# Kernel optimization log

Measured on AMD Instinct MI355X. Metric: run time of the kernel, lower is better.

## Reference

```python
import jax, jax.numpy as jnp
import numpy as np

RADIUS = 3
DIAM = 2 * RADIUS + 1  # 7
NP = DIAM * DIAM       # 49 taps


def _cubic(d, a=-0.75):
    # torch bicubic kernel (a = -0.75)
    d = np.abs(d)
    return np.where(d <= 1, (a + 2) * d**3 - (a + 3) * d**2 + 1,
                    np.where(d < 2, a * d**3 - 5 * a * d**2 + 8 * a * d - 4 * a, 0.0))


def _resize_matrix(out_size, in_size):
    # dense [out,in] matrix reproducing torch F.interpolate bicubic, align_corners=False
    i = np.arange(out_size)
    x = (i + 0.5) * in_size / out_size - 0.5
    x0 = np.floor(x).astype(np.int64)
    t = x - x0
    W = np.zeros((out_size, in_size), np.float32)
    for k in range(-1, 3):
        w = _cubic(t - k)
        idx = np.clip(x0 + k, 0, in_size - 1)  # border replicate
        np.add.at(W, (i, idx), w.astype(np.float32))
    return jnp.asarray(W)


def _bicubic(x, GH, GW):
    B, C, H, W = x.shape
    Wh = _resize_matrix(GH, H)
    Ww = _resize_matrix(GW, W)
    return jnp.einsum('Hh,bchw,Ww->bcHW', Wh, x, Ww)


def _jbu(source, guidance, w1, b1, w2, b2, temp, sigma):
    # FeatUp JBULearnedRange.forward (eval mode: Dropout2d is identity)
    B, _, GH, GW = guidance.shape
    # range_proj: 1x1 conv -> GELU -> 1x1 conv
    q = jnp.einsum('kc,bchw->bkhw', w1, guidance) + b1[None, :, None, None]
    q = jax.nn.gelu(q, approximate=False)
    q = jnp.einsum('kc,bchw->bkhw', w2, q) + b2[None, :, None, None]  # [B,32,GH,GW]
    qp = jnp.pad(q, ((0, 0), (0, 0), (RADIUS, RADIUS), (RADIUS, RADIUS)), mode='reflect')
    # scores[b,p,h,w] = <key at center, key at offset p> (avoids B*32*49*H*W unfold)
    scores = jnp.stack([jnp.sum(qp[:, :, di:di + GH, dj:dj + GW] * q, axis=1)
                        for di in range(DIAM) for dj in range(DIAM)], axis=1)  # [B,49,GH,GW]
    t = jnp.clip(jnp.exp(temp), 1e-4, 1e4)
    range_kernel = jax.nn.softmax(t * scores, axis=1)
    dist = jnp.linspace(-1.0, 1.0, DIAM)
    gy, gx = jnp.meshgrid(dist, dist, indexing='ij')
    spatial_kernel = jnp.exp(-(gy**2 + gx**2) / (2.0 * sigma**2)).reshape(1, NP, 1, 1)
    k = range_kernel * spatial_kernel
    k = k / jnp.clip(jnp.sum(k, axis=1, keepdims=True), 1e-7, None)
    hr = _bicubic(source, GH, GW)
    hrp = jnp.pad(hr, ((0, 0), (0, 0), (RADIUS, RADIUS), (RADIUS, RADIUS)), mode='reflect')
    # AdaptiveConv: per-pixel 7x7 kernel applied to all channels
    out = jnp.zeros_like(hr)
    p_idx = 0
    for di in range(DIAM):
        for dj in range(DIAM):
            out = out + hrp[:, :, di:di + GH, dj:dj + GW] * k[:, p_idx][:, None]
            p_idx += 1
    return out


def _forward(x, guidance, linear_w, linear_b, w1s, b1s, w2s, b2s, temps, sigmas):
    f = (x @ linear_w.T + linear_b).reshape(-1, 3, 18, 18)
    for i in range(4):  # up1..up4, each fed the FULL guidance as in the Decoder
        f = _jbu(f, guidance, w1s[i], b1s[i], w2s[i], b2s[i], temps[i], sigmas[i])
    return f


def setup_inputs() -> dict:
    key = jax.random.key(0)
    ks = jax.random.split(key, 6)
    B = 8
    return {
        'x': jax.random.normal(ks[0], (B, 1000), jnp.float32),
        'guidance': jax.random.uniform(ks[1], (B, 3, 224, 224), jnp.float32),
        'linear_w': jax.random.normal(ks[2], (972, 1000), jnp.float32) * 0.03,
        'linear_b': jnp.zeros((972,), jnp.float32),
        'w1s': jax.random.normal(ks[3], (4, 32, 3), jnp.float32) * 0.1,
        'b1s': jnp.zeros((4, 32), jnp.float32),
        'w2s': jax.random.normal(ks[4], (4, 32, 32), jnp.float32) * 0.1,
        'b2s': jnp.zeros((4, 32), jnp.float32),
        'temps': jnp.zeros((4,), jnp.float32),   # range_temp init 0.0
        'sigmas': jnp.ones((4,), jnp.float32),   # sigma_spatial init 1.0
    }


def reference(x, guidance, linear_w, linear_b, w1s, b1s, w2s, b2s, temps, sigmas):
    return _forward(x, guidance, linear_w, linear_b, w1s, b1s, w2s, b2s, temps, sigmas)
```

## Files before the change

kernel.cpp:

```cpp
#include <hip/hip_runtime.h>
#include <hip/hip_fp16.h>
#include <math.h>

#define GHH 224
#define GWW 224
#define HW (GHH*GWW)
#define BATCH 8
#define RAD 3
#define DIAM 7
#define NPTS 49
#define QC 32
#define TILE 16
#define TP (TILE + 2*RAD)
#define TPIX (TP*TP)
#define CS 485
#define SQ_B 31040

typedef _Float16 h2 __attribute__((ext_vector_type(2)));
typedef _Float16 v8h __attribute__((ext_vector_type(8)));
typedef float v4f __attribute__((ext_vector_type(4)));

#if defined(__has_builtin)
#if __has_builtin(__builtin_amdgcn_fdot2)
#define HAS_FDOT2 1
#endif
#endif

__device__ __forceinline__ h2 as_h2(float f) { union { float f; h2 h; } u; u.f = f; return u.h; }

__device__ __forceinline__ float dot2acc(float a, float b, float acc) {
#ifdef HAS_FDOT2
    return __builtin_amdgcn_fdot2(as_h2(a), as_h2(b), acc, false);
#else
    union { float f; __half2 h; } ua, ub; ua.f = a; ub.f = b;
    float2 fa = __half22float2(ua.h), fb = __half22float2(ub.h);
    return acc + fa.x * fb.x + fa.y * fb.y;
#endif
}

__device__ __forceinline__ float dot16(const float4& a, const float4& b, float acc) {
    acc = dot2acc(a.x, b.x, acc);
    acc = dot2acc(a.y, b.y, acc);
    acc = dot2acc(a.z, b.z, acc);
    acc = dot2acc(a.w, b.w, acc);
    return acc;
}

__device__ __forceinline__ int refl(int i) {
    if (i < 0) i = -i;
    if (i >= GHH) i = 2 * GHH - 2 - i;
    return i;
}

__device__ __forceinline__ float gelu_fast(float v) {
    float u = 0.7978845608f * v * (1.f + 0.044715f * v * v);
    float e = __expf(2.f * u);
    float th = 1.f - 2.f / (e + 1.f);
    return 0.5f * v * (1.f + th);
}

__global__ void linear_prep_kernel(const float* __restrict__ x,
                                   const float* __restrict__ W,
                                   const float* __restrict__ bias,
                                   float* __restrict__ f0,
                                   const float* __restrict__ w2s,
                                   __half* __restrict__ wsB,
                                   const float* __restrict__ w1s,
                                   const float* __restrict__ b1s,
                                   __half* __restrict__ wsW1,
                                   const float* __restrict__ guid,
                                   float4* __restrict__ guid4) {
    int blk = blockIdx.x;
    if (blk >= 1946) {
        int i = (blk - 1946) * 256 + threadIdx.x;
        int b = i / HW, pix = i % HW;
        guid4[i] = make_float4(guid[(b * 3) * HW + pix],
                               guid[(b * 3 + 1) * HW + pix],
                               guid[(b * 3 + 2) * HW + pix], 0.f);
        return;
    }
    if (blk == 1945) {
        int tid = threadIdx.x;
        if (tid < 128) {
            int s = tid >> 5, c = tid & 31;
            wsW1[tid * 4 + 0] = __float2half(w1s[s * 96 + c * 3 + 0]);
            wsW1[tid * 4 + 1] = __float2half(w1s[s * 96 + c * 3 + 1]);
            wsW1[tid * 4 + 2] = __float2half(w1s[s * 96 + c * 3 + 2]);
            wsW1[tid * 4 + 3] = __float2half(b1s[s * 32 + c]);
        }
        return;
    }
    if (blk == 1944) {
        int tid = threadIdx.x;
        int s = tid >> 6, l = tid & 63;
        int n0 = l & 15, kq = l >> 4;
        const float* w2 = w2s + s * 1024;
        __half* dst = wsB + (size_t)tid * 16;
        #pragma unroll
        for (int j = 0; j < 8; j++) {
            dst[j]     = __float2half(w2[n0 * QC + kq * 8 + j]);
            dst[8 + j] = __float2half(w2[(n0 + 16) * QC + kq * 8 + j]);
        }
        return;
    }
    int gwave = (blk * blockDim.x + threadIdx.x) >> 6;
    int lane = threadIdx.x & 63;
    if (gwave >= BATCH * 972) return;
    int b = gwave / 972, j = gwave % 972;
    const float* xr = x + b * 1000;
    const float* wr = W + j * 1000;
    float s = 0.f;
    for (int k = lane; k < 1000; k += 64)
        s += xr[k] * wr[k];
    #pragma unroll
    for (int off = 32; off; off >>= 1) s += __shfl_down(s, off, 64);
    if (lane == 0) f0[gwave] = s + bias[j];
}

__device__ __forceinline__ float cubicw(float d) {
    d = fabsf(d);
    if (d <= 1.f) return ((1.25f * d - 2.25f) * d) * d + 1.f;
    if (d < 2.f)  return ((-0.75f * d + 3.75f) * d - 6.f) * d + 3.f;
    return 0.f;
}

__global__ void bicubic_kernel(const float* __restrict__ f0, float4* __restrict__ hr4) {
    int idx = blockIdx.x * blockDim.x + threadIdx.x;
    if (idx >= BATCH * HW) return;
    int pix = idx % HW;
    int b = idx / HW;
    int w = pix % GWW, h = pix / GWW;
    float xx = (w + 0.5f) * (18.f / 224.f) - 0.5f;
    float yy = (h + 0.5f) * (18.f / 224.f) - 0.5f;
    float fx0 = floorf(xx), fy0 = floorf(yy);
    int x0 = (int)fx0, y0 = (int)fy0;
    float tx = xx - fx0, ty = yy - fy0;
    float wx[4], wy[4];
    int ix[4], iy[4];
    #pragma unroll
    for (int k = 0; k < 4; k++) {
        wx[k] = cubicw(tx - (float)(k - 1));
        wy[k] = cubicw(ty - (float)(k - 1));
        int a = x0 + (k - 1); ix[k] = min(max(a, 0), 17);
        a = y0 + (k - 1);     iy[k] = min(max(a, 0), 17);
    }
    float acc[3];
    #pragma unroll
    for (int c = 0; c < 3; c++) {
        const float* src = f0 + (b * 3 + c) * 324;
        float a = 0.f;
        #pragma unroll
        for (int ky = 0; ky < 4; ky++) {
            float rowv = 0.f;
            #pragma unroll
            for (int kx = 0; kx < 4; kx++) rowv += wx[kx] * src[iy[ky] * 18 + ix[kx]];
            a += wy[ky] * rowv;
        }
        acc[c] = a;
    }
    hr4[idx] = make_float4(acc[0], acc[1], acc[2], 0.f);
}

__global__ __launch_bounds__(256, 4) void jbu_kernel(
    const float4* __restrict__ guid4,
    const __half* __restrict__ wsW1,
    const __half* __restrict__ wsB, const float* __restrict__ b2,
    const float4* __restrict__ hr4,
    float4* __restrict__ out4,
    float* __restrict__ outP,
    const float* __restrict__ temps,
    const float* __restrict__ sigmas,
    int stage)
{
    __shared__ __align__(16) char smem[SQ_B + TPIX * 16];
    float4* sq = (float4*)smem;
    float4* sh = (float4*)(smem + SQ_B);

    const int tx = threadIdx.x, ty = threadIdx.y;
    const int tid = ty * TILE + tx;
    const int b = blockIdx.z;
    const int h0 = blockIdx.y * TILE, w0 = blockIdx.x * TILE;

    const bool interior = (h0 >= RAD) && (h0 + TILE + RAD <= GHH) &&
                          (w0 >= RAD) && (w0 + TILE + RAD <= GWW);
    if (interior) {
        const float4* hb = hr4 + (size_t)b * HW + (size_t)(h0 - RAD) * GWW + (w0 - RAD);
        for (int i = tid; i < TPIX; i += 256) {
            int r = i / TP, cx = i % TP;
            sh[i] = hb[(size_t)r * GWW + cx];
        }
    } else {
        for (int i = tid; i < TPIX; i += 256) {
            int r = i / TP, cx = i % TP;
            int gh = refl(h0 - RAD + r);
            int gw = refl(w0 - RAD + cx);
            sh[i] = hr4[(size_t)b * HW + (size_t)gh * GWW + gw];
        }
    }

    const int w = tid >> 6, l = tid & 63;
    const int n0 = l & 15, kq = l >> 4;
    const v8h* Bp = (const v8h*)(wsB + ((size_t)stage * 64 + l) * 16);
    const v8h B0 = Bp[0], B1 = Bp[1];
    const float bias0 = b2[n0], bias1 = b2[n0 + 16];
    union { _Float16 h[32]; float4 f4[4]; } W1;
    {
        const float4* wp = (const float4*)(wsW1 + stage * 128 + kq * 32);
        W1.f4[0] = wp[0]; W1.f4[1] = wp[1]; W1.f4[2] = wp[2]; W1.f4[3] = wp[3];
    }

    #pragma unroll 1
    for (int r2 = 0; r2 < 2; r2++) {
        #pragma unroll
        for (int tt = 0; tt < 4; tt++) {
            int base = r2 * 256 + w * 64 + tt * 16;
            int p = base + n0;
            int pc = min(p, TPIX - 1);
            int rr = pc / TP, cc = pc - rr * TP;
            int gh = refl(h0 - RAD + rr), gw = refl(w0 - RAD + cc);
            float4 g = guid4[(size_t)b * HW + (size_t)gh * GWW + gw];
            union { _Float16 h[8]; v8h v; } A;
            #pragma unroll
            for (int j = 0; j < 8; j++) {
                float vv = fmaf((float)W1.h[j * 4], g.x,
                           fmaf((float)W1.h[j * 4 + 1], g.y,
                           fmaf((float)W1.h[j * 4 + 2], g.z, (float)W1.h[j * 4 + 3])));
                A.h[j] = (_Float16)gelu_fast(vv);
            }
            v4f D0 = {0.f, 0.f, 0.f, 0.f}, D1 = {0.f, 0.f, 0.f, 0.f};
            D0 = __builtin_amdgcn_mfma_f32_16x16x32_f16(A.v, B0, D0, 0, 0, 0);
            D1 = __builtin_amdgcn_mfma_f32_16x16x32_f16(A.v, B1, D1, 0, 0, 0);
            #pragma unroll
            for (int r = 0; r < 4; r++) {
                int gpx = base + 4 * kq + r;
                if (gpx < TPIX) {
                    *(_Float16*)(smem + ((n0 >> 3) * CS + gpx) * 16 + (n0 & 7) * 2)
                        = (_Float16)(D0[r] + bias0);
                    *(_Float16*)(smem + (((n0 >> 3) + 2) * CS + gpx) * 16 + (n0 & 7) * 2)
                        = (_Float16)(D1[r] + bias1);
                }
            }
        }
    }
    __syncthreads();

    int ci = (ty + RAD) * TP + tx + RAD;
    float4 c0 = sq[ci], c1 = sq[CS + ci], c2 = sq[2 * CS + ci], c3 = sq[3 * CS + ci];

    float s[NPTS];
    int p = 0;
    #pragma unroll
    for (int di = 0; di < DIAM; di++) {
        int rb = (ty + di) * TP + tx;
        #pragma unroll
        for (int dj = 0; dj < DIAM; dj++, p++) {
            int ni = rb + dj;
            float acc = dot16(c0, sq[ni], 0.f);
            acc = dot16(c1, sq[CS + ni], acc);
            acc = dot16(c2, sq[2 * CS + ni], acc);
            acc = dot16(c3, sq[3 * CS + ni], acc);
            s[p] = acc;
        }
    }

    float t = __expf(temps[stage]);
    t = fminf(fmaxf(t, 1e-4f), 1e4f);
    float sig = sigmas[stage];
    float inv2s2 = 1.f / (2.f * sig * sig);
    float m = -1e30f;
    #pragma unroll
    for (int p2 = 0; p2 < NPTS; p2++) { s[p2] *= t; m = fmaxf(m, s[p2]); }
    float den = 0.f;
    #pragma unroll
    for (int p2 = 0; p2 < NPTS; p2++) { s[p2] = __expf(s[p2] - m); den += s[p2]; }
    float rden = 1.f / den;
    float ksum = 0.f;
    #pragma unroll
    for (int p2 = 0; p2 < NPTS; p2++) {
        int di = p2 / 7, dj = p2 % 7;
        float dy = (float)(di - 3) * (1.f / 3.f);
        float dx = (float)(dj - 3) * (1.f / 3.f);
        float spat = __expf(-(dy * dy + dx * dx) * inv2s2);
        s[p2] = s[p2] * rden * spat;
        ksum += s[p2];
    }
    float rk = 1.f / fmaxf(ksum, 1e-7f);

    float o0 = 0.f, o1 = 0.f, o2 = 0.f;
    p = 0;
    #pragma unroll
    for (int di = 0; di < DIAM; di++) {
        int rb = (ty + di) * TP + tx;
        #pragma unroll
        for (int dj = 0; dj < DIAM; dj++, p++) {
            float4 hv = sh[rb + dj];
            float kp = s[p] * rk;
            o0 += kp * hv.x;
            o1 += kp * hv.y;
            o2 += kp * hv.z;
        }
    }
    if (stage < 3) {
        out4[(size_t)b * HW + (size_t)(h0 + ty) * GWW + (w0 + tx)] = make_float4(o0, o1, o2, 0.f);
    } else {
        size_t obase = (size_t)b * 3 * HW + (size_t)(h0 + ty) * GWW + (w0 + tx);
        outP[obase]          = o0;
        outP[obase + HW]     = o1;
        outP[obase + 2 * HW] = o2;
    }
}

extern "C" void kernel_launch(void* const* d_in, const int* in_sizes, int n_in,
                              void* d_out, int out_size, void* d_ws, size_t ws_size,
                              hipStream_t stream) {
    const float* x      = (const float*)d_in[0];
    const float* guid   = (const float*)d_in[1];
    const float* lw     = (const float*)d_in[2];
    const float* lb     = (const float*)d_in[3];
    const float* w1s    = (const float*)d_in[4];
    const float* b1s    = (const float*)d_in[5];
    const float* w2s    = (const float*)d_in[6];
    const float* b2s    = (const float*)d_in[7];
    const float* temps  = (const float*)d_in[8];
    const float* sigmas = (const float*)d_in[9];

    char* ws = (char*)d_ws;
    const size_t P4_BYTES = (size_t)BATCH * HW * sizeof(float4);
    float4* guid4 = (float4*)ws;
    float4* hr4A  = (float4*)(ws + P4_BYTES);
    float4* hr4B  = (float4*)(ws + 2 * P4_BYTES);
    float*  f0    = (float*)(ws + 3 * P4_BYTES);
    __half* wsB   = (__half*)(ws + 3 * P4_BYTES + 31104);
    __half* wsW1  = (__half*)(ws + 3 * P4_BYTES + 31104 + 8192);

    linear_prep_kernel<<<1946 + 1568, 256, 0, stream>>>(
        x, lw, lb, f0, w2s, wsB, w1s, b1s, wsW1, guid, guid4);
    bicubic_kernel<<<(BATCH * HW + 255) / 256, 256, 0, stream>>>(f0, hr4A);

    dim3 jgrid(14, 14, BATCH), jblock(16, 16);
    const float4* hins[4]  = { hr4A, hr4B, hr4A, hr4B };
    float4*       fouts[4] = { hr4B, hr4A, hr4B, nullptr };
    for (int s = 0; s < 4; s++) {
        jbu_kernel<<<jgrid, jblock, 0, stream>>>(
            guid4, wsW1, wsB, b2s + s * 32,
            hins[s], fouts[s], (s == 3) ? (float*)d_out : nullptr,
            temps, sigmas, s);
    }
}
```

Before: 294.3 us.

## Compute two pixels per thread with 16x32 tiles and single-pass softmax

Each JBU block now covers a 16x32 tile, and each thread produces two horizontally adjacent output pixels. Each thread loads every shared-memory neighbour key and source value once and uses it for both pixels. The halo is stored in an even/odd column-interleaved layout so adjacent threads touch consecutive slots. The softmax, spatial-kernel normalisation and weighted sum are fused into one streaming pass. This drops the 49-entry score array and the max subtraction by folding the softmax denominator into the clamp, which risks overflow in exp(t*s) for large scores. The bigger tile needs more shared memory and registers, and launch bounds are lowered to 2 blocks per CU.

```diff
diff --git a/kernel.cpp b/kernel.cpp
--- a/kernel.cpp
+++ b/kernel.cpp
@@ -8,13 +8,15 @@
 #define BATCH 8
 #define RAD 3
 #define DIAM 7
-#define NPTS 49
 #define QC 32
-#define TILE 16
-#define TP (TILE + 2*RAD)
-#define TPIX (TP*TP)
-#define CS 485
-#define SQ_B 31040
+#define TH 16
+#define TW 32
+#define QTH (TH + 2*RAD)
+#define QTW (TW + 2*RAD)
+#define QR 40
+#define QP 882
+#define QPIX (QTH*QTW)
+#define SQ_B (4*QP*16)
 
 typedef _Float16 h2 __attribute__((ext_vector_type(2)));
 typedef _Float16 v8h __attribute__((ext_vector_type(8)));
@@ -161,7 +163,7 @@
     hr4[idx] = make_float4(acc[0], acc[1], acc[2], 0.f);
 }
 
-__global__ __launch_bounds__(256, 4) void jbu_kernel(
+__global__ __launch_bounds__(256, 2) void jbu_kernel(
     const float4* __restrict__ guid4,
     const __half* __restrict__ wsW1,
     const __half* __restrict__ wsB, const float* __restrict__ b2,
@@ -172,29 +174,30 @@
     const float* __restrict__ sigmas,
     int stage)
 {
-    __shared__ __align__(16) char smem[SQ_B + TPIX * 16];
+    __shared__ __align__(16) char smem[SQ_B + QTH * QR * 16];
     float4* sq = (float4*)smem;
     float4* sh = (float4*)(smem + SQ_B);
 
     const int tx = threadIdx.x, ty = threadIdx.y;
-    const int tid = ty * TILE + tx;
+    const int tid = ty * 16 + tx;
     const int b = blockIdx.z;
-    const int h0 = blockIdx.y * TILE, w0 = blockIdx.x * TILE;
-
-    const bool interior = (h0 >= RAD) && (h0 + TILE + RAD <= GHH) &&
-                          (w0 >= RAD) && (w0 + TILE + RAD <= GWW);
+    const int h0 = blockIdx.y * TH, w0 = blockIdx.x * TW;
+
+    const bool interior = (h0 >= RAD) && (h0 + TH + RAD <= GHH) &&
+                          (w0 >= RAD) && (w0 + TW + RAD <= GWW);
+
     if (interior) {
         const float4* hb = hr4 + (size_t)b * HW + (size_t)(h0 - RAD) * GWW + (w0 - RAD);
-        for (int i = tid; i < TPIX; i += 256) {
-            int r = i / TP, cx = i % TP;
-            sh[i] = hb[(size_t)r * GWW + cx];
+        for (int i = tid; i < QPIX; i += 256) {
+            int r = i / QTW, c = i - r * QTW;
+            sh[r * QR + (c >> 1) + (c & 1) * 19] = hb[(size_t)r * GWW + c];
         }
     } else {
-        for (int i = tid; i < TPIX; i += 256) {
-            int r = i / TP, cx = i % TP;
+        for (int i = tid; i < QPIX; i += 256) {
+            int r = i / QTW, c = i - r * QTW;
             int gh = refl(h0 - RAD + r);
-            int gw = refl(w0 - RAD + cx);
-            sh[i] = hr4[(size_t)b * HW + (size_t)gh * GWW + gw];
+            int gw = refl(w0 - RAD + c);
+            sh[r * QR + (c >> 1) + (c & 1) * 19] = hr4[(size_t)b * HW + (size_t)gh * GWW + gw];
         }
     }
 
@@ -210,13 +213,14 @@
     }
 
     #pragma unroll 1
-    for (int r2 = 0; r2 < 2; r2++) {
+    for (int r2 = 0; r2 < 4; r2++) {
         #pragma unroll
         for (int tt = 0; tt < 4; tt++) {
             int base = r2 * 256 + w * 64 + tt * 16;
+            if (base >= QPIX) break;
             int p = base + n0;
-            int pc = min(p, TPIX - 1);
-            int rr = pc / TP, cc = pc - rr * TP;
+            int pc = min(p, QPIX - 1);
+            int rr = pc / QTW, cc = pc - rr * QTW;
             int gh = refl(h0 - RAD + rr), gw = refl(w0 - RAD + cc);
             float4 g = guid4[(size_t)b * HW + (size_t)gh * GWW + gw];
             union { _Float16 h[8]; v8h v; } A;
@@ -233,10 +237,12 @@
             #pragma unroll
             for (int r = 0; r < 4; r++) {
                 int gpx = base + 4 * kq + r;
-                if (gpx < TPIX) {
-                    *(_Float16*)(smem + ((n0 >> 3) * CS + gpx) * 16 + (n0 & 7) * 2)
+                if (gpx < QPIX) {
+                    int rr2 = gpx / QTW, cc2 = gpx - rr2 * QTW;
+                    int slot = rr2 * QR + (cc2 >> 1) + (cc2 & 1) * 19;
+                    *(_Float16*)(smem + ((n0 >> 3) * QP + slot) * 16 + (n0 & 7) * 2)
                         = (_Float16)(D0[r] + bias0);
-                    *(_Float16*)(smem + (((n0 >> 3) + 2) * CS + gpx) * 16 + (n0 & 7) * 2)
+                    *(_Float16*)(smem + (((n0 >> 3) + 2) * QP + slot) * 16 + (n0 & 7) * 2)
                         = (_Float16)(D1[r] + bias1);
                 }
             }
@@ -244,22 +250,13 @@
     }
     __syncthreads();
 
-    int ci = (ty + RAD) * TP + tx + RAD;
-    float4 c0 = sq[ci], c1 = sq[CS + ci], c2 = sq[2 * CS + ci], c3 = sq[3 * CS + ci];
-
-    float s[NPTS];
-    int p = 0;
-    #pragma unroll
-    for (int di = 0; di < DIAM; di++) {
-        int rb = (ty + di) * TP + tx;
-        #pragma unroll
-        for (int dj = 0; dj < DIAM; dj++, p++) {
-            int ni = rb + dj;
-            float acc = dot16(c0, sq[ni], 0.f);
-            acc = dot16(c1, sq[CS + ni], acc);
-            acc = dot16(c2, sq[2 * CS + ni], acc);
-            acc = dot16(c3, sq[3 * CS + ni], acc);
-            s[p] = acc;
+    float4 A0c[4], A1c[4];
+    {
+        int rbc = (ty + RAD) * QR;
+        #pragma unroll
+        for (int c = 0; c < 4; c++) {
+            A0c[c] = sq[c * QP + rbc + tx + 20];
+            A1c[c] = sq[c * QP + rbc + tx + 2];
         }
     }
 
@@ -267,46 +264,59 @@
     t = fminf(fmaxf(t, 1e-4f), 1e4f);
     float sig = sigmas[stage];
     float inv2s2 = 1.f / (2.f * sig * sig);
-    float m = -1e30f;
-    #pragma unroll
-    for (int p2 = 0; p2 < NPTS; p2++) { s[p2] *= t; m = fmaxf(m, s[p2]); }
-    float den = 0.f;
-    #pragma unroll
-    for (int p2 = 0; p2 < NPTS; p2++) { s[p2] = __expf(s[p2] - m); den += s[p2]; }
-    float rden = 1.f / den;
-    float ksum = 0.f;
-    #pragma unroll
-    for (int p2 = 0; p2 < NPTS; p2++) {
-        int di = p2 / 7, dj = p2 % 7;
-        float dy = (float)(di - 3) * (1.f / 3.f);
-        float dx = (float)(dj - 3) * (1.f / 3.f);
-        float spat = __expf(-(dy * dy + dx * dx) * inv2s2);
-        s[p2] = s[p2] * rden * spat;
-        ksum += s[p2];
-    }
-    float rk = 1.f / fmaxf(ksum, 1e-7f);
-
-    float o0 = 0.f, o1 = 0.f, o2 = 0.f;
-    p = 0;
+    float sd[DIAM];
+    #pragma unroll
+    for (int i = 0; i < DIAM; i++) {
+        float d = (float)(i - 3) * (1.f / 3.f);
+        sd[i] = __expf(-d * d * inv2s2);
+    }
+
+    float es0 = 0.f, ws0 = 0.f, n00 = 0.f, n01 = 0.f, n02 = 0.f;
+    float es1 = 0.f, ws1 = 0.f, n10 = 0.f, n11 = 0.f, n12 = 0.f;
     #pragma unroll
     for (int di = 0; di < DIAM; di++) {
-        int rb = (ty + di) * TP + tx;
-        #pragma unroll
-        for (int dj = 0; dj < DIAM; dj++, p++) {
-            float4 hv = sh[rb + dj];
-            float kp = s[p] * rk;
-            o0 += kp * hv.x;
-            o1 += kp * hv.y;
-            o2 += kp * hv.z;
-        }
-    }
+        const int rb = (ty + di) * QR + tx;
+        const float sy = sd[di];
+        #pragma unroll
+        for (int dj = 0; dj < 8; dj++) {
+            const int SOFF = (dj >> 1) + (dj & 1) * 19;
+            const int ni = rb + SOFF;
+            float4 v0 = sq[ni], v1 = sq[QP + ni], v2 = sq[2 * QP + ni], v3 = sq[3 * QP + ni];
+            float4 hv = sh[ni];
+            if (dj < 7) {
+                float s = dot16(A0c[0], v0, 0.f);
+                s = dot16(A0c[1], v1, s);
+                s = dot16(A0c[2], v2, s);
+                s = dot16(A0c[3], v3, s);
+                float e = __expf(t * s);
+                float wgt = e * sy * sd[dj];
+                es0 += e; ws0 += wgt;
+                n00 += wgt * hv.x; n01 += wgt * hv.y; n02 += wgt * hv.z;
+            }
+            if (dj > 0) {
+                float s = dot16(A1c[0], v0, 0.f);
+                s = dot16(A1c[1], v1, s);
+                s = dot16(A1c[2], v2, s);
+                s = dot16(A1c[3], v3, s);
+                float e = __expf(t * s);
+                float wgt = e * sy * sd[dj - 1];
+                es1 += e; ws1 += wgt;
+                n10 += wgt * hv.x; n11 += wgt * hv.y; n12 += wgt * hv.z;
+            }
+        }
+    }
+    float r0 = 1.f / fmaxf(ws0, 1e-7f * es0);
+    float r1 = 1.f / fmaxf(ws1, 1e-7f * es1);
+
     if (stage < 3) {
-        out4[(size_t)b * HW + (size_t)(h0 + ty) * GWW + (w0 + tx)] = make_float4(o0, o1, o2, 0.f);
+        size_t obase = (size_t)b * HW + (size_t)(h0 + ty) * GWW + (w0 + 2 * tx);
+        out4[obase]     = make_float4(n00 * r0, n01 * r0, n02 * r0, 0.f);
+        out4[obase + 1] = make_float4(n10 * r1, n11 * r1, n12 * r1, 0.f);
     } else {
-        size_t obase = (size_t)b * 3 * HW + (size_t)(h0 + ty) * GWW + (w0 + tx);
-        outP[obase]          = o0;
-        outP[obase + HW]     = o1;
-        outP[obase + 2 * HW] = o2;
+        size_t obase = (size_t)b * 3 * HW + (size_t)(h0 + ty) * GWW + (w0 + 2 * tx);
+        *(float2*)&outP[obase]          = make_float2(n00 * r0, n10 * r1);
+        *(float2*)&outP[obase + HW]     = make_float2(n01 * r0, n11 * r1);
+        *(float2*)&outP[obase + 2 * HW] = make_float2(n02 * r0, n12 * r1);
     }
 }
 
@@ -337,7 +347,7 @@
         x, lw, lb, f0, w2s, wsB, w1s, b1s, wsW1, guid, guid4);
     bicubic_kernel<<<(BATCH * HW + 255) / 256, 256, 0, stream>>>(f0, hr4A);
 
-    dim3 jgrid(14, 14, BATCH), jblock(16, 16);
+    dim3 jgrid(GWW / TW, GHH / TH, BATCH), jblock(16, 16);
     const float4* hins[4]  = { hr4A, hr4B, hr4A, hr4B };
     float4*       fouts[4] = { hr4B, hr4A, hr4B, nullptr };
     for (int s = 0; s < 4; s++) {
```

New measurement: 335.7 us. +14.1%, slower.

## Fuse scoring, softmax and aggregation in one pass; vectorize MFMA key stores

Applied to the files above, without the earlier changes.

The 49-entry score array and its three separate passes (max, exp/sum, spatial weighting) are replaced by a single fused loop. That loop computes each dot product, exponentiates without subtracting a max, applies a separable spatial weight and accumulates the output, normalizing once at the end. The MFMA operands are swapped so each lane holds four consecutive channels of one pixel, which allows packed 8-byte LDS stores instead of scalar half stores. This is meant to cut register pressure, instruction count and LDS store traffic. Dropping the max subtraction risks exp overflow if temperature times score becomes large.

```diff
diff --git a/kernel.cpp b/kernel.cpp
--- a/kernel.cpp
+++ b/kernel.cpp
@@ -8,7 +8,6 @@
 #define BATCH 8
 #define RAD 3
 #define DIAM 7
-#define NPTS 49
 #define QC 32
 #define TILE 16
 #define TP (TILE + 2*RAD)
@@ -201,13 +200,16 @@
     const int w = tid >> 6, l = tid & 63;
     const int n0 = l & 15, kq = l >> 4;
     const v8h* Bp = (const v8h*)(wsB + ((size_t)stage * 64 + l) * 16);
-    const v8h B0 = Bp[0], B1 = Bp[1];
-    const float bias0 = b2[n0], bias1 = b2[n0 + 16];
+    const v8h W2a = Bp[0], W2b = Bp[1];
+    const float4 b2a = *(const float4*)(b2 + 4 * kq);
+    const float4 b2b = *(const float4*)(b2 + 16 + 4 * kq);
     union { _Float16 h[32]; float4 f4[4]; } W1;
     {
         const float4* wp = (const float4*)(wsW1 + stage * 128 + kq * 32);
         W1.f4[0] = wp[0]; W1.f4[1] = wp[1]; W1.f4[2] = wp[2]; W1.f4[3] = wp[3];
     }
+    const int plane0 = kq >> 1;
+    const int boff   = (kq & 1) * 8;
 
     #pragma unroll 1
     for (int r2 = 0; r2 < 2; r2++) {
@@ -228,17 +230,20 @@
                 A.h[j] = (_Float16)gelu_fast(vv);
             }
             v4f D0 = {0.f, 0.f, 0.f, 0.f}, D1 = {0.f, 0.f, 0.f, 0.f};
-            D0 = __builtin_amdgcn_mfma_f32_16x16x32_f16(A.v, B0, D0, 0, 0, 0);
-            D1 = __builtin_amdgcn_mfma_f32_16x16x32_f16(A.v, B1, D1, 0, 0, 0);
-            #pragma unroll
-            for (int r = 0; r < 4; r++) {
-                int gpx = base + 4 * kq + r;
-                if (gpx < TPIX) {
-                    *(_Float16*)(smem + ((n0 >> 3) * CS + gpx) * 16 + (n0 & 7) * 2)
-                        = (_Float16)(D0[r] + bias0);
-                    *(_Float16*)(smem + (((n0 >> 3) + 2) * CS + gpx) * 16 + (n0 & 7) * 2)
-                        = (_Float16)(D1[r] + bias1);
-                }
+            D0 = __builtin_amdgcn_mfma_f32_16x16x32_f16(W2a, A.v, D0, 0, 0, 0);
+            D1 = __builtin_amdgcn_mfma_f32_16x16x32_f16(W2b, A.v, D1, 0, 0, 0);
+            if (p < TPIX) {
+                union { _Float16 h[4]; uint2 u; } q0, q1;
+                q0.h[0] = (_Float16)(D0[0] + b2a.x);
+                q0.h[1] = (_Float16)(D0[1] + b2a.y);
+                q0.h[2] = (_Float16)(D0[2] + b2a.z);
+                q0.h[3] = (_Float16)(D0[3] + b2a.w);
+                q1.h[0] = (_Float16)(D1[0] + b2b.x);
+                q1.h[1] = (_Float16)(D1[1] + b2b.y);
+                q1.h[2] = (_Float16)(D1[2] + b2b.z);
+                q1.h[3] = (_Float16)(D1[3] + b2b.w);
+                *(uint2*)(smem + (plane0 * CS + p) * 16 + boff)       = q0.u;
+                *(uint2*)(smem + ((2 + plane0) * CS + p) * 16 + boff) = q1.u;
             }
         }
     }
@@ -246,67 +251,47 @@
 
     int ci = (ty + RAD) * TP + tx + RAD;
     float4 c0 = sq[ci], c1 = sq[CS + ci], c2 = sq[2 * CS + ci], c3 = sq[3 * CS + ci];
-
-    float s[NPTS];
-    int p = 0;
-    #pragma unroll
-    for (int di = 0; di < DIAM; di++) {
-        int rb = (ty + di) * TP + tx;
-        #pragma unroll
-        for (int dj = 0; dj < DIAM; dj++, p++) {
-            int ni = rb + dj;
-            float acc = dot16(c0, sq[ni], 0.f);
-            acc = dot16(c1, sq[CS + ni], acc);
-            acc = dot16(c2, sq[2 * CS + ni], acc);
-            acc = dot16(c3, sq[3 * CS + ni], acc);
-            s[p] = acc;
-        }
-    }
 
     float t = __expf(temps[stage]);
     t = fminf(fmaxf(t, 1e-4f), 1e4f);
     float sig = sigmas[stage];
     float inv2s2 = 1.f / (2.f * sig * sig);
-    float m = -1e30f;
-    #pragma unroll
-    for (int p2 = 0; p2 < NPTS; p2++) { s[p2] *= t; m = fmaxf(m, s[p2]); }
-    float den = 0.f;
-    #pragma unroll
-    for (int p2 = 0; p2 < NPTS; p2++) { s[p2] = __expf(s[p2] - m); den += s[p2]; }
-    float rden = 1.f / den;
-    float ksum = 0.f;
-    #pragma unroll
-    for (int p2 = 0; p2 < NPTS; p2++) {
-        int di = p2 / 7, dj = p2 % 7;
-        float dy = (float)(di - 3) * (1.f / 3.f);
-        float dx = (float)(dj - 3) * (1.f / 3.f);
-        float spat = __expf(-(dy * dy + dx * dx) * inv2s2);
-        s[p2] = s[p2] * rden * spat;
-        ksum += s[p2];
-    }
-    float rk = 1.f / fmaxf(ksum, 1e-7f);
-
-    float o0 = 0.f, o1 = 0.f, o2 = 0.f;
-    p = 0;
+    float sd[DIAM];
+    #pragma unroll
+    for (int i = 0; i < DIAM; i++) {
+        float d = (float)(i - 3) * (1.f / 3.f);
+        sd[i] = __expf(-d * d * inv2s2);
+    }
+
+    float es = 0.f, wsum = 0.f, o0 = 0.f, o1 = 0.f, o2 = 0.f;
     #pragma unroll
     for (int di = 0; di < DIAM; di++) {
         int rb = (ty + di) * TP + tx;
+        float sy = sd[di];
         #pragma unroll
-        for (int dj = 0; dj < DIAM; dj++, p++) {
-            float4 hv = sh[rb + dj];
-            float kp = s[p] * rk;
-            o0 += kp * hv.x;
-            o1 += kp * hv.y;
-            o2 += kp * hv.z;
-        }
-    }
+        for (int dj = 0; dj < DIAM; dj++) {
+            int ni = rb + dj;
+            float s = dot16(c0, sq[ni], 0.f);
+            s = dot16(c1, sq[CS + ni], s);
+            s = dot16(c2, sq[2 * CS + ni], s);
+            s = dot16(c3, sq[3 * CS + ni], s);
+            float4 hv = sh[ni];
+            float e = __expf(t * s);
+            float wgt = e * sy * sd[dj];
+            es += e; wsum += wgt;
+            o0 += wgt * hv.x; o1 += wgt * hv.y; o2 += wgt * hv.z;
+        }
+    }
+    float rk = 1.f / fmaxf(wsum, 1e-7f * es);
+
     if (stage < 3) {
-        out4[(size_t)b * HW + (size_t)(h0 + ty) * GWW + (w0 + tx)] = make_float4(o0, o1, o2, 0.f);
+        out4[(size_t)b * HW + (size_t)(h0 + ty) * GWW + (w0 + tx)] =
+            make_float4(o0 * rk, o1 * rk, o2 * rk, 0.f);
     } else {
         size_t obase = (size_t)b * 3 * HW + (size_t)(h0 + ty) * GWW + (w0 + tx);
-        outP[obase]          = o0;
-        outP[obase + HW]     = o1;
-        outP[obase + 2 * HW] = o2;
+        outP[obase]          = o0 * rk;
+        outP[obase + HW]     = o1 * rk;
+        outP[obase + 2 * HW] = o2 * rk;
     }
 }
 
```

Measured after the change: 279.5 us. 5.0% less time.
